# Kernel optimization log

Hardware: AMD Instinct MI355X
Metric: run time of the kernel (lower is better)

The kernel has to match this reference:

```python
import jax, jax.numpy as jnp
import numpy as np

N, E = 100000, 1600000
IN_C, HID, OUT_C, EDGE_D, GRAPH_D = 32, 32, 8, 16, 16

def _lin_w(key, fan_in, fan_out):
    return jax.random.normal(key, (fan_in, fan_out), dtype=jnp.float32) * (1.0 / np.sqrt(fan_in))

def setup_inputs() -> dict:
    key = jax.random.key(0)
    ks = jax.random.split(key, 12)
    return {
        "x": jax.random.uniform(ks[0], (N, IN_C), dtype=jnp.float32),
        "edge_attr": jax.random.uniform(ks[1], (E, EDGE_D), dtype=jnp.float32),
        "graph_attr": jax.random.uniform(ks[2], (1, GRAPH_D), dtype=jnp.float32),
        "edge_index": jax.random.randint(ks[3], (2, E), 0, N, dtype=jnp.int32),
        "batch": jnp.zeros((N,), dtype=jnp.int32),
        "W_node": _lin_w(ks[4], IN_C, HID),
        "b_node": jnp.zeros((HID,), jnp.float32),
        "W_graph": _lin_w(ks[5], GRAPH_D, GRAPH_D),
        "b_graph": jnp.zeros((GRAPH_D,), jnp.float32),
        "W_edge_agg": _lin_w(ks[6], 2 * HID + EDGE_D + GRAPH_D, EDGE_D),
        "b_edge_agg": jnp.zeros((EDGE_D,), jnp.float32),
        "W_node_agg": _lin_w(ks[7], EDGE_D + HID + GRAPH_D, HID),
        "b_node_agg": jnp.zeros((HID,), jnp.float32),
        "W_sage_l": _lin_w(ks[8], HID, OUT_C),
        "b_sage_l": jnp.zeros((OUT_C,), jnp.float32),
        "W_sage_r": _lin_w(ks[9], HID, OUT_C),
    }

def _seg_mean(vals, idx, num_segments):
    # scatter-mean: sum per segment / count (count clamped to 1 for empty segments)
    sums = jax.ops.segment_sum(vals, idx, num_segments=num_segments)
    cnt = jax.ops.segment_sum(jnp.ones((vals.shape[0],), vals.dtype), idx, num_segments=num_segments)
    return sums / jnp.maximum(cnt, 1.0)[:, None]

def reference(x, edge_attr, graph_attr, edge_index, batch,
              W_node, b_node, W_graph, b_graph,
              W_edge_agg, b_edge_agg, W_node_agg, b_node_agg,
              W_sage_l, b_sage_l, W_sage_r):
    n = x.shape[0]
    row, col = edge_index[0], edge_index[1]
    # node / graph embeddings (plain linear, no activation)
    h_i = x @ W_node + b_node                       # [N, HID]
    h_G = graph_attr @ W_graph + b_graph            # [1, GRAPH_D]
    h_G_e = jnp.broadcast_to(h_G, (row.shape[0], h_G.shape[1]))
    # edge aggregator: gather both endpoints, concat, linear, relu
    edge_in = jnp.concatenate([h_i[row], h_i[col], edge_attr, h_G_e], axis=-1)  # [E, 96]
    h_edge_agg = jax.nn.relu(edge_in @ W_edge_agg + b_edge_agg)                 # [E, EDGE_D]
    # per-node mean of edges whose source == node (replaces O(N*E) python loop)
    m_N = _seg_mean(h_edge_agg, row, n)             # [N, EDGE_D]
    # node aggregator
    h_G_n = jnp.broadcast_to(h_G, (n, h_G.shape[1]))
    h_i2 = jax.nn.relu(jnp.concatenate([h_i, m_N, h_G_n], axis=-1) @ W_node_agg + b_node_agg)
    # SAGEConv (mean aggr): out = lin_l(mean_{j->i} x_j) + lin_r(x_i)
    agg = _seg_mean(h_i2[row], col, n)
    h_nodes = agg @ W_sage_l + b_sage_l + h_i2 @ W_sage_r  # [N, OUT_C]
    # global mean pool over batch assignment (single graph here)
    pooled = _seg_mean(h_nodes, batch, 1)           # [1, OUT_C]
    return jax.nn.log_softmax(pooled, axis=1)
```

## Files before the change

### kernel.cpp

```cpp
#include <hip/hip_runtime.h>
#include <hip/hip_fp16.h>
#include <hip/hip_fp8.h>

#define HID 32
#define IN_C 32
#define EDGE_D 16
#define GRAPH_D 16
#define OUT_C 8
#define STRIDE 48
#define SLOT_B 32

__device__ __forceinline__ unsigned char f32_to_fp8(float f) {
    __hip_fp8_e4m3 v(f);
    return (unsigned char)v.__x;
}
__device__ __forceinline__ float fp8_to_f32(unsigned char b) {
    __hip_fp8_e4m3 v;
    v.__x = (__hip_fp8_storage_t)b;
    return (float)v;
}

__global__ void __launch_bounds__(256)
k_node_emb(const float* __restrict__ x,
           const float* __restrict__ W,
           const float* __restrict__ b,
           const float* __restrict__ graph_attr,
           const float* __restrict__ W_graph,
           const float* __restrict__ b_graph,
           const float* __restrict__ W_edge_agg,
           const float* __restrict__ b_edge_agg,
           const float* __restrict__ W_node_agg,
           const float* __restrict__ b_node_agg,
           float* __restrict__ bias_edge,
           float* __restrict__ bias_node,
           int* __restrict__ zero_base, int zero_count,
           __half* __restrict__ h,
           unsigned char* __restrict__ Pr,
           unsigned char* __restrict__ Pc, int n) {
    __shared__ float hG[GRAPH_D];
    int t = threadIdx.x;
    for (int idx = blockIdx.x * blockDim.x + t; idx < zero_count;
         idx += gridDim.x * blockDim.x)
        zero_base[idx] = 0;

    if (blockIdx.x == 0 && t < GRAPH_D) {
        float acc = b_graph[t];
        for (int d = 0; d < GRAPH_D; d++)
            acc += graph_attr[d] * W_graph[d * GRAPH_D + t];
        hG[t] = acc;
    }
    __syncthreads();
    if (blockIdx.x == 0) {
        if (t < EDGE_D) {
            float acc = b_edge_agg[t];
            for (int d = 0; d < GRAPH_D; d++)
                acc += hG[d] * W_edge_agg[(2 * HID + EDGE_D + d) * EDGE_D + t];
            bias_edge[t] = acc;
        }
        if (t < HID) {
            float acc = b_node_agg[t];
            for (int d = 0; d < GRAPH_D; d++)
                acc += hG[d] * W_node_agg[(HID + EDGE_D + d) * HID + t];
            bias_node[t] = acc;
        }
    }

    int i = blockIdx.x * blockDim.x + t;
    if (i >= n) return;
    float in[IN_C];
    const float4* xr = (const float4*)(x + (size_t)i * IN_C);
#pragma unroll
    for (int q = 0; q < IN_C / 4; q++) {
        float4 v = xr[q];
        in[4 * q + 0] = v.x; in[4 * q + 1] = v.y;
        in[4 * q + 2] = v.z; in[4 * q + 3] = v.w;
    }
    float acc[HID];
#pragma unroll
    for (int j = 0; j < HID; j++) acc[j] = b[j];
#pragma unroll
    for (int k = 0; k < IN_C; k++) {
        float a = in[k];
#pragma unroll
        for (int j = 0; j < HID; j++) acc[j] += a * W[k * HID + j];
    }
    float4 packed[4];
    __half2* ph = (__half2*)packed;
#pragma unroll
    for (int j = 0; j < 16; j++)
        ph[j] = __floats2half2_rn(acc[2 * j], acc[2 * j + 1]);
    float4* hr = (float4*)(h + (size_t)i * HID);
#pragma unroll
    for (int q = 0; q < 4; q++) hr[q] = packed[q];

    float pr[EDGE_D], pc[EDGE_D];
#pragma unroll
    for (int j = 0; j < EDGE_D; j++) { pr[j] = 0.f; pc[j] = 0.f; }
#pragma unroll
    for (int k = 0; k < HID; k++) {
        float a = acc[k];
#pragma unroll
        for (int j = 0; j < EDGE_D; j++) {
            pr[j] += a * W_edge_agg[k * EDGE_D + j];
            pc[j] += a * W_edge_agg[(HID + k) * EDGE_D + j];
        }
    }
    unsigned char pb[EDGE_D];
#pragma unroll
    for (int j = 0; j < EDGE_D; j++) pb[j] = f32_to_fp8(pr[j]);
    *(uint4*)(Pr + (size_t)i * EDGE_D) = *(const uint4*)pb;
#pragma unroll
    for (int j = 0; j < EDGE_D; j++) pb[j] = f32_to_fp8(pc[j]);
    *(uint4*)(Pc + (size_t)i * EDGE_D) = *(const uint4*)pb;
}

__global__ void __launch_bounds__(256)
k_edge_place(const int* __restrict__ ei,
             const unsigned char* __restrict__ Pr,
             const unsigned char* __restrict__ Pc,
             const float* __restrict__ ea,
             const float* __restrict__ We,
             const float* __restrict__ biasE,
             int* __restrict__ cur_row,
             int* __restrict__ cur_col,
             unsigned char* __restrict__ he_bucket, int E) {
    int e = blockIdx.x * blockDim.x + threadIdx.x;
    if (e >= E) return;
    int r = ei[e];
    int c = ei[E + e];

    uint4 g = *(const uint4*)(Pr + (size_t)r * EDGE_D);
    uint4 q = *(const uint4*)(Pc + (size_t)c * EDGE_D);
    float eav[EDGE_D];
    {
        const float4* er = (const float4*)(ea + (size_t)e * EDGE_D);
#pragma unroll
        for (int k = 0; k < 4; k++) {
            float4 v = er[k];
            eav[4 * k + 0] = v.x; eav[4 * k + 1] = v.y;
            eav[4 * k + 2] = v.z; eav[4 * k + 3] = v.w;
        }
    }
    int pr = atomicAdd(cur_row + r, 1);
    atomicAdd(cur_col + c, 1);

    float acc[EDGE_D];
    {
        const unsigned char* gb = (const unsigned char*)&g;
        const unsigned char* qb = (const unsigned char*)&q;
#pragma unroll
        for (int j = 0; j < EDGE_D; j++)
            acc[j] = biasE[j] + fp8_to_f32(gb[j]) + fp8_to_f32(qb[j]);
    }
#pragma unroll
    for (int k = 0; k < EDGE_D; k++) {
        float a = eav[k];
#pragma unroll
        for (int j = 0; j < EDGE_D; j++)
            acc[j] += a * We[(2 * HID + k) * EDGE_D + j];
    }

    if (pr < STRIDE) {
        unsigned char hb[16];
#pragma unroll
        for (int j = 0; j < EDGE_D; j++)
            hb[j] = f32_to_fp8(fmaxf(acc[j], 0.f));
        uint4 w0 = *(const uint4*)hb;
        uint4 w1; w1.x = (unsigned int)c; w1.y = 0; w1.z = 0; w1.w = 0;
        unsigned char* dst = he_bucket + ((size_t)r * STRIDE + pr) * SLOT_B;
        *(uint4*)dst = w0;
        *(uint4*)(dst + 16) = w1;
    }
}

#define RNODES 128
__global__ void __launch_bounds__(256)
k_reduce(const __half* __restrict__ hi,
         const unsigned char* __restrict__ he_bucket,
         const int* __restrict__ cur_row,
         const int* __restrict__ cur_col,
         const int* __restrict__ batch,
         const float* __restrict__ Wna,
         const float* __restrict__ biasN,
         float* __restrict__ Vg,
         float* __restrict__ Wg,
         float* __restrict__ ncnt, int n) {
    __shared__ float ms_s[RNODES][EDGE_D + 1];
    __shared__ float s_s[RNODES];
    __shared__ int cnt_s[RNODES];
    __shared__ float vpart[4][HID];
    __shared__ float wpart[4][HID];
    __shared__ float redc[4];
    int tid = threadIdx.x;
    int g = tid >> 4;
    int l = tid & 15;
    int base = blockIdx.x * RNODES;

    if (tid < RNODES)
        cnt_s[tid] = (base + tid < n) ? cur_row[base + tid] : 0;
    __syncthreads();

    for (int iter = 0; iter < RNODES / 16; iter++) {
        int node = base + iter * 16 + g;
        int cnt = cnt_s[iter * 16 + g];
        int d = cnt < STRIDE ? cnt : STRIDE;
        float inv = 1.0f / fmaxf((float)cnt, 1.0f);
        float a16[EDGE_D];
#pragma unroll
        for (int j = 0; j < EDGE_D; j++) a16[j] = 0.f;
        float sw = 0.f;
        const unsigned char* bb = he_bucket + (size_t)node * STRIDE * SLOT_B;
        for (int t = l; t < d; t += 16) {
            uint4 q0 = *(const uint4*)(bb + (size_t)t * SLOT_B);
            int col = *(const int*)(bb + (size_t)t * SLOT_B + 16);
            int ic = cur_col[col];
            sw += 1.0f / fmaxf((float)ic, 1.0f);
            const unsigned char* qb = (const unsigned char*)&q0;
#pragma unroll
            for (int j = 0; j < EDGE_D; j++)
                a16[j] += fp8_to_f32(qb[j]);
        }
#pragma unroll
        for (int m = 8; m >= 1; m >>= 1) {
#pragma unroll
            for (int k = 0; k < m; k++) {
                float send = (l & m) ? a16[k] : a16[k + m];
                float recv = __shfl_xor(send, m, 16);
                float keep = (l & m) ? a16[k + m] : a16[k];
                a16[k] = keep + recv;
            }
        }
#pragma unroll
        for (int m = 1; m <= 8; m <<= 1) sw += __shfl_xor(sw, m, 16);
        ms_s[iter * 16 + g][l] = a16[0] * inv;
        if (l == 0) s_s[iter * 16 + g] = sw;
    }
    __syncthreads();

    int i = base + tid;
    float vv[HID];
    float h2[HID];
#pragma unroll
    for (int j = 0; j < HID; j++) { vv[j] = 0.f; h2[j] = 0.f; }
    float cc = 0.f;

    if (tid < RNODES && i < n) {
        float ms[EDGE_D];
#pragma unroll
        for (int k = 0; k < EDGE_D; k++) ms[k] = ms_s[tid][k];
        float sv = s_s[tid];

        float hr[HID];
        {
            float4 t[4];
            const float4* hrow = (const float4*)(hi + (size_t)i * HID);
#pragma unroll
            for (int q = 0; q < 4; q++) t[q] = hrow[q];
            const __half2* hp = (const __half2*)t;
#pragma unroll
            for (int j = 0; j < 16; j++) {
                float2 f = __half22float2(hp[j]);
                hr[2 * j] = f.x; hr[2 * j + 1] = f.y;
            }
        }
#pragma unroll
        for (int j = 0; j < HID; j++) h2[j] = biasN[j];
#pragma unroll
        for (int k = 0; k < HID; k++) {
            float a = hr[k];
#pragma unroll
            for (int j = 0; j < HID; j++) h2[j] += a * Wna[k * HID + j];
        }
#pragma unroll
        for (int k = 0; k < EDGE_D; k++) {
            float a = ms[k];
#pragma unroll
            for (int j = 0; j < HID; j++) h2[j] += a * Wna[(HID + k) * HID + j];
        }
#pragma unroll
        for (int j = 0; j < HID; j++) h2[j] = fmaxf(h2[j], 0.f);

#pragma unroll
        for (int j = 0; j < HID; j++) vv[j] = sv * h2[j];

        if (batch[i] == 0) cc = 1.f;
        else {
#pragma unroll
            for (int j = 0; j < HID; j++) h2[j] = 0.f;
        }
    }

#pragma unroll
    for (int k = 0; k < HID; k++) {
        vv[k] += __shfl_xor(vv[k], 32, 64);
        h2[k] += __shfl_xor(h2[k], 32, 64);
    }
    int l32 = tid & 31;
#pragma unroll
    for (int m = 16; m >= 1; m >>= 1) {
#pragma unroll
        for (int k = 0; k < m; k++) {
            {
                float send = (l32 & m) ? vv[k] : vv[k + m];
                float recv = __shfl_xor(send, m, 32);
                float keep = (l32 & m) ? vv[k + m] : vv[k];
                vv[k] = keep + recv;
            }
            {
                float send = (l32 & m) ? h2[k] : h2[k + m];
                float recv = __shfl_xor(send, m, 32);
                float keep = (l32 & m) ? h2[k + m] : h2[k];
                h2[k] = keep + recv;
            }
        }
    }
    int w = tid >> 6;
    if ((tid & 63) < 32) {
        vpart[w][l32] = vv[0];
        wpart[w][l32] = h2[0];
    }
#pragma unroll
    for (int off = 32; off > 0; off >>= 1) cc += __shfl_down(cc, off, 64);
    if ((tid & 63) == 0) redc[w] = cc;
    __syncthreads();
    if (tid < HID) {
        atomicAdd(Vg + tid, vpart[0][tid] + vpart[1][tid] + vpart[2][tid] + vpart[3][tid]);
    } else if (tid < 2 * HID) {
        int j = tid - HID;
        atomicAdd(Wg + j, wpart[0][j] + wpart[1][j] + wpart[2][j] + wpart[3][j]);
    } else if (tid == 2 * HID) {
        atomicAdd(ncnt, redc[0] + redc[1] + redc[2] + redc[3]);
    }
}

__global__ void k_final(const float* __restrict__ Vg,
                        const float* __restrict__ Wg,
                        const float* __restrict__ ncnt,
                        const float* __restrict__ Wsl,
                        const float* __restrict__ Wsr,
                        const float* __restrict__ bsl,
                        float* __restrict__ out) {
    if (threadIdx.x == 0 && blockIdx.x == 0) {
        float c = fmaxf(ncnt[0], 1.0f);
        float p[OUT_C];
        float m = -1e30f;
#pragma unroll
        for (int j = 0; j < OUT_C; j++) p[j] = 0.f;
        for (int k = 0; k < HID; k++) {
            float v = Vg[k], w = Wg[k];
#pragma unroll
            for (int j = 0; j < OUT_C; j++)
                p[j] += v * Wsl[k * OUT_C + j] + w * Wsr[k * OUT_C + j];
        }
#pragma unroll
        for (int j = 0; j < OUT_C; j++) {
            p[j] = p[j] / c + bsl[j];
            m = fmaxf(m, p[j]);
        }
        float s = 0.f;
#pragma unroll
        for (int j = 0; j < OUT_C; j++) s += expf(p[j] - m);
        float l = logf(s);
#pragma unroll
        for (int j = 0; j < OUT_C; j++) out[j] = p[j] - m - l;
    }
}

extern "C" void kernel_launch(void* const* d_in, const int* in_sizes, int n_in,
                              void* d_out, int out_size, void* d_ws, size_t ws_size,
                              hipStream_t stream) {
    const float* x          = (const float*)d_in[0];
    const float* edge_attr  = (const float*)d_in[1];
    const float* graph_attr = (const float*)d_in[2];
    const int*   edge_index = (const int*)d_in[3];
    const int*   batch      = (const int*)d_in[4];
    const float* W_node     = (const float*)d_in[5];
    const float* b_node     = (const float*)d_in[6];
    const float* W_graph    = (const float*)d_in[7];
    const float* b_graph    = (const float*)d_in[8];
    const float* W_edge_agg = (const float*)d_in[9];
    const float* b_edge_agg = (const float*)d_in[10];
    const float* W_node_agg = (const float*)d_in[11];
    const float* b_node_agg = (const float*)d_in[12];
    const float* W_sage_l   = (const float*)d_in[13];
    const float* b_sage_l   = (const float*)d_in[14];
    const float* W_sage_r   = (const float*)d_in[15];

    const int n = in_sizes[0] / IN_C;
    const int E = in_sizes[3] / 2;

    char* wsb = (char*)d_ws;
    int*  cur_row = (int*)wsb;
    int*  cur_col = cur_row + n;
    float* Vg     = (float*)(cur_col + n);
    float* Wg     = Vg + HID;
    float* ncnt   = Wg + HID;
    int   zero_count = 2 * n + 80;
    size_t off = (size_t)zero_count * 4;
    unsigned char* he_bucket = (unsigned char*)(wsb + off);
    off += (size_t)n * STRIDE * SLOT_B;
    __half* h_i  = (__half*)(wsb + off); off += (size_t)n * HID * 2;
    float* biasE = (float*)(wsb + off);  off += 16 * 4;
    float* biasN = (float*)(wsb + off);  off += HID * 4;
    unsigned char* Pr = (unsigned char*)(wsb + off); off += (size_t)n * EDGE_D;
    unsigned char* Pc = (unsigned char*)(wsb + off); off += (size_t)n * EDGE_D;

    k_node_emb<<<(n + 255) / 256, 256, 0, stream>>>(x, W_node, b_node,
                                                    graph_attr, W_graph, b_graph,
                                                    W_edge_agg, b_edge_agg,
                                                    W_node_agg, b_node_agg,
                                                    biasE, biasN,
                                                    cur_row, zero_count, h_i,
                                                    Pr, Pc, n);

    k_edge_place<<<(E + 255) / 256, 256, 0, stream>>>(edge_index, Pr, Pc, edge_attr,
                                                      W_edge_agg, biasE,
                                                      cur_row, cur_col,
                                                      he_bucket, E);

    k_reduce<<<(n + RNODES - 1) / RNODES, 256, 0, stream>>>(h_i, he_bucket,
                                                            cur_row, cur_col,
                                                            batch, W_node_agg,
                                                            biasN, Vg, Wg, ncnt, n);

    k_final<<<1, 64, 0, stream>>>(Vg, Wg, ncnt, W_sage_l, W_sage_r,
                                  b_sage_l, (float*)d_out);
}
```

Baseline: 503.9 us.

## Precompute h_i·W_node_agg in node kernel and reduce via shared memory

The node embedding kernel now stores h_i·W_node_agg[0:HID] (in fp16) instead of h_i, which moves the 32x32 matvec out of the reduce kernel. The reduce kernel adds only the bias and the m_N contribution. Its cross-lane shuffle transpose reduction is replaced by a shared-memory staging of h2 with a per-channel sum over 8 partial groups. This removes shuffle-heavy work and register pressure from k_reduce. The cost is extra compute in k_node_emb and fp16 rounding applied after the matvec rather than before.

After: 503.1 us. No clear change (-0.2%).

```diff
diff --git a/kernel.cpp b/kernel.cpp
--- a/kernel.cpp
+++ b/kernel.cpp
@@ -34,7 +34,7 @@
            float* __restrict__ bias_edge,
            float* __restrict__ bias_node,
            int* __restrict__ zero_base, int zero_count,
-           __half* __restrict__ h,
+           __half* __restrict__ An,
            unsigned char* __restrict__ Pr,
            unsigned char* __restrict__ Pc, int n) {
     __shared__ float hG[GRAPH_D];
@@ -84,34 +84,48 @@
 #pragma unroll
         for (int j = 0; j < HID; j++) acc[j] += a * W[k * HID + j];
     }
-    float4 packed[4];
-    __half2* ph = (__half2*)packed;
-#pragma unroll
-    for (int j = 0; j < 16; j++)
-        ph[j] = __floats2half2_rn(acc[2 * j], acc[2 * j + 1]);
-    float4* hr = (float4*)(h + (size_t)i * HID);
-#pragma unroll
-    for (int q = 0; q < 4; q++) hr[q] = packed[q];
-
-    float pr[EDGE_D], pc[EDGE_D];
-#pragma unroll
-    for (int j = 0; j < EDGE_D; j++) { pr[j] = 0.f; pc[j] = 0.f; }
-#pragma unroll
-    for (int k = 0; k < HID; k++) {
-        float a = acc[k];
-#pragma unroll
-        for (int j = 0; j < EDGE_D; j++) {
-            pr[j] += a * W_edge_agg[k * EDGE_D + j];
-            pc[j] += a * W_edge_agg[(HID + k) * EDGE_D + j];
-        }
-    }
-    unsigned char pb[EDGE_D];
-#pragma unroll
-    for (int j = 0; j < EDGE_D; j++) pb[j] = f32_to_fp8(pr[j]);
-    *(uint4*)(Pr + (size_t)i * EDGE_D) = *(const uint4*)pb;
-#pragma unroll
-    for (int j = 0; j < EDGE_D; j++) pb[j] = f32_to_fp8(pc[j]);
-    *(uint4*)(Pc + (size_t)i * EDGE_D) = *(const uint4*)pb;
+
+    {
+        float pr[EDGE_D], pc[EDGE_D];
+#pragma unroll
+        for (int j = 0; j < EDGE_D; j++) { pr[j] = 0.f; pc[j] = 0.f; }
+#pragma unroll
+        for (int k = 0; k < HID; k++) {
+            float a = acc[k];
+#pragma unroll
+            for (int j = 0; j < EDGE_D; j++) {
+                pr[j] += a * W_edge_agg[k * EDGE_D + j];
+                pc[j] += a * W_edge_agg[(HID + k) * EDGE_D + j];
+            }
+        }
+        unsigned char pb[EDGE_D];
+#pragma unroll
+        for (int j = 0; j < EDGE_D; j++) pb[j] = f32_to_fp8(pr[j]);
+        *(uint4*)(Pr + (size_t)i * EDGE_D) = *(const uint4*)pb;
+#pragma unroll
+        for (int j = 0; j < EDGE_D; j++) pb[j] = f32_to_fp8(pc[j]);
+        *(uint4*)(Pc + (size_t)i * EDGE_D) = *(const uint4*)pb;
+    }
+
+    {
+        float an[HID];
+#pragma unroll
+        for (int j = 0; j < HID; j++) an[j] = 0.f;
+#pragma unroll
+        for (int k = 0; k < HID; k++) {
+            float a = acc[k];
+#pragma unroll
+            for (int j = 0; j < HID; j++) an[j] += a * W_node_agg[k * HID + j];
+        }
+        float4 packed[4];
+        __half2* ph = (__half2*)packed;
+#pragma unroll
+        for (int j = 0; j < 16; j++)
+            ph[j] = __floats2half2_rn(an[2 * j], an[2 * j + 1]);
+        float4* dst = (float4*)(An + (size_t)i * HID);
+#pragma unroll
+        for (int q = 0; q < 4; q++) dst[q] = packed[q];
+    }
 }
 
 __global__ void __launch_bounds__(256)
@@ -175,7 +189,7 @@
 
 #define RNODES 128
 __global__ void __launch_bounds__(256)
-k_reduce(const __half* __restrict__ hi,
+k_reduce(const __half* __restrict__ An,
          const unsigned char* __restrict__ he_bucket,
          const int* __restrict__ cur_row,
          const int* __restrict__ cur_col,
@@ -188,9 +202,11 @@
     __shared__ float ms_s[RNODES][EDGE_D + 1];
     __shared__ float s_s[RNODES];
     __shared__ int cnt_s[RNODES];
-    __shared__ float vpart[4][HID];
-    __shared__ float wpart[4][HID];
-    __shared__ float redc[4];
+    __shared__ float h2_s[RNODES][HID + 1];
+    __shared__ float sv_s[RNODES];
+    __shared__ float vq[8][HID];
+    __shared__ float wq[8][HID];
+    __shared__ float redc[2];
     int tid = threadIdx.x;
     int g = tid >> 4;
     int l = tid & 15;
@@ -238,98 +254,78 @@
     __syncthreads();
 
     int i = base + tid;
-    float vv[HID];
-    float h2[HID];
-#pragma unroll
-    for (int j = 0; j < HID; j++) { vv[j] = 0.f; h2[j] = 0.f; }
     float cc = 0.f;
-
-    if (tid < RNODES && i < n) {
-        float ms[EDGE_D];
-#pragma unroll
-        for (int k = 0; k < EDGE_D; k++) ms[k] = ms_s[tid][k];
-        float sv = s_s[tid];
-
-        float hr[HID];
-        {
-            float4 t[4];
-            const float4* hrow = (const float4*)(hi + (size_t)i * HID);
-#pragma unroll
-            for (int q = 0; q < 4; q++) t[q] = hrow[q];
-            const __half2* hp = (const __half2*)t;
+    if (tid < RNODES) {
+        float h2[HID];
+        float sv = 0.f;
+        if (i < n) {
+            float4 t4[4];
+            const float4* arow = (const float4*)(An + (size_t)i * HID);
+#pragma unroll
+            for (int q = 0; q < 4; q++) t4[q] = arow[q];
+            const __half2* hp = (const __half2*)t4;
 #pragma unroll
             for (int j = 0; j < 16; j++) {
                 float2 f = __half22float2(hp[j]);
-                hr[2 * j] = f.x; hr[2 * j + 1] = f.y;
+                h2[2 * j]     = f.x + biasN[2 * j];
+                h2[2 * j + 1] = f.y + biasN[2 * j + 1];
             }
-        }
-#pragma unroll
-        for (int j = 0; j < HID; j++) h2[j] = biasN[j];
-#pragma unroll
-        for (int k = 0; k < HID; k++) {
-            float a = hr[k];
-#pragma unroll
-            for (int j = 0; j < HID; j++) h2[j] += a * Wna[k * HID + j];
-        }
-#pragma unroll
-        for (int k = 0; k < EDGE_D; k++) {
-            float a = ms[k];
-#pragma unroll
-            for (int j = 0; j < HID; j++) h2[j] += a * Wna[(HID + k) * HID + j];
-        }
-#pragma unroll
-        for (int j = 0; j < HID; j++) h2[j] = fmaxf(h2[j], 0.f);
-
-#pragma unroll
-        for (int j = 0; j < HID; j++) vv[j] = sv * h2[j];
-
-        if (batch[i] == 0) cc = 1.f;
-        else {
+#pragma unroll
+            for (int k = 0; k < EDGE_D; k++) {
+                float a = ms_s[tid][k];
+#pragma unroll
+                for (int j = 0; j < HID; j++)
+                    h2[j] += a * Wna[(HID + k) * HID + j];
+            }
+#pragma unroll
+            for (int j = 0; j < HID; j++) h2[j] = fmaxf(h2[j], 0.f);
+            if (batch[i] == 0) { cc = 1.f; sv = s_s[tid]; }
+            else {
+#pragma unroll
+                for (int j = 0; j < HID; j++) h2[j] = 0.f;
+            }
+        } else {
 #pragma unroll
             for (int j = 0; j < HID; j++) h2[j] = 0.f;
         }
-    }
-
-#pragma unroll
-    for (int k = 0; k < HID; k++) {
-        vv[k] += __shfl_xor(vv[k], 32, 64);
-        h2[k] += __shfl_xor(h2[k], 32, 64);
-    }
-    int l32 = tid & 31;
-#pragma unroll
-    for (int m = 16; m >= 1; m >>= 1) {
-#pragma unroll
-        for (int k = 0; k < m; k++) {
-            {
-                float send = (l32 & m) ? vv[k] : vv[k + m];
-                float recv = __shfl_xor(send, m, 32);
-                float keep = (l32 & m) ? vv[k + m] : vv[k];
-                vv[k] = keep + recv;
-            }
-            {
-                float send = (l32 & m) ? h2[k] : h2[k + m];
-                float recv = __shfl_xor(send, m, 32);
-                float keep = (l32 & m) ? h2[k + m] : h2[k];
-                h2[k] = keep + recv;
-            }
-        }
-    }
-    int w = tid >> 6;
-    if ((tid & 63) < 32) {
-        vpart[w][l32] = vv[0];
-        wpart[w][l32] = h2[0];
+#pragma unroll
+        for (int j = 0; j < HID; j++) h2_s[tid][j] = h2[j];
+        sv_s[tid] = sv;
+    }
+    __syncthreads();
+
+    {
+        int ch = tid & 31;
+        int q  = tid >> 5;
+        float vsum = 0.f, wsum = 0.f;
+        int nb = q * 16;
+#pragma unroll
+        for (int t2 = 0; t2 < 16; t2++) {
+            float hval = h2_s[nb + t2][ch];
+            float sval = sv_s[nb + t2];
+            vsum += sval * hval;
+            wsum += hval;
+        }
+        vq[q][ch] = vsum;
+        wq[q][ch] = wsum;
     }
 #pragma unroll
     for (int off = 32; off > 0; off >>= 1) cc += __shfl_down(cc, off, 64);
-    if ((tid & 63) == 0) redc[w] = cc;
+    if ((tid & 63) == 0 && tid < RNODES) redc[tid >> 6] = cc;
     __syncthreads();
     if (tid < HID) {
-        atomicAdd(Vg + tid, vpart[0][tid] + vpart[1][tid] + vpart[2][tid] + vpart[3][tid]);
+        float v = 0.f;
+#pragma unroll
+        for (int q = 0; q < 8; q++) v += vq[q][tid];
+        atomicAdd(Vg + tid, v);
     } else if (tid < 2 * HID) {
         int j = tid - HID;
-        atomicAdd(Wg + j, wpart[0][j] + wpart[1][j] + wpart[2][j] + wpart[3][j]);
+        float w = 0.f;
+#pragma unroll
+        for (int q = 0; q < 8; q++) w += wq[q][j];
+        atomicAdd(Wg + j, w);
     } else if (tid == 2 * HID) {
-        atomicAdd(ncnt, redc[0] + redc[1] + redc[2] + redc[3]);
+        atomicAdd(ncnt, redc[0] + redc[1]);
     }
 }
 
@@ -399,7 +395,7 @@
     size_t off = (size_t)zero_count * 4;
     unsigned char* he_bucket = (unsigned char*)(wsb + off);
     off += (size_t)n * STRIDE * SLOT_B;
-    __half* h_i  = (__half*)(wsb + off); off += (size_t)n * HID * 2;
+    __half* An   = (__half*)(wsb + off); off += (size_t)n * HID * 2;
     float* biasE = (float*)(wsb + off);  off += 16 * 4;
     float* biasN = (float*)(wsb + off);  off += HID * 4;
     unsigned char* Pr = (unsigned char*)(wsb + off); off += (size_t)n * EDGE_D;
@@ -410,7 +406,7 @@
                                                     W_edge_agg, b_edge_agg,
                                                     W_node_agg, b_node_agg,
                                                     biasE, biasN,
-                                                    cur_row, zero_count, h_i,
+                                                    cur_row, zero_count, An,
                                                     Pr, Pc, n);
 
     k_edge_place<<<(E + 255) / 256, 256, 0, stream>>>(edge_index, Pr, Pc, edge_attr,
@@ -418,7 +414,7 @@
                                                       cur_row, cur_col,
                                                       he_bucket, E);
 
-    k_reduce<<<(n + RNODES - 1) / RNODES, 256, 0, stream>>>(h_i, he_bucket,
+    k_reduce<<<(n + RNODES - 1) / RNODES, 256, 0, stream>>>(An, he_bucket,
                                                             cur_row, cur_col,
                                                             batch, W_node_agg,
                                                             biasN, Vg, Wg, ncnt, n);
```
